# Kernel optimization log

Hardware: AMD Instinct MI355X
Metric: run time of the kernel (lower is better)

## Reference

```python
import jax, jax.numpy as jnp
import numpy as np

EPS_BN = 1e-5  # torch BatchNorm1d default eps
EPS_W = 1e-8   # dist reciprocal eps from source


def _bn_relu(x, gamma, beta):
    # x: [B, C, N]; training-mode batchnorm (biased var over B and N per channel)
    mean = jnp.mean(x, axis=(0, 2), keepdims=True)
    var = jnp.mean((x - mean) ** 2, axis=(0, 2), keepdims=True)
    xn = (x - mean) * jax.lax.rsqrt(var + EPS_BN)
    return jax.nn.relu(xn * gamma[None, :, None] + beta[None, :, None])


def setup_inputs() -> dict:
    key = jax.random.key(0)
    ks = jax.random.split(key, 12)
    B, N, S, D = 2, 16384, 4096, 256
    mlp = [256, 256]
    in_ch = 2 * D
    inp = {
        'xyz1': jax.random.normal(ks[0], (B, 3, N), jnp.float32),
        'xyz2': jax.random.normal(ks[1], (B, 3, S), jnp.float32),
        'points1': jax.random.normal(ks[2], (B, D, N), jnp.float32),
        'points2': jax.random.normal(ks[3], (B, D, S), jnp.float32),
    }
    last = in_ch
    for i, out in enumerate(mlp):
        inp[f'W{i}'] = jax.random.normal(ks[4 + 2 * i], (out, last), jnp.float32) * (1.0 / np.sqrt(last))
        inp[f'b{i}'] = jnp.zeros((out,), jnp.float32)
        inp[f'g{i}'] = jnp.ones((out,), jnp.float32)
        inp[f'be{i}'] = jnp.zeros((out,), jnp.float32)
        last = out
    return inp


def reference(xyz1, xyz2, points1, points2, W0, b0, g0, be0, W1, b1, g1, be1):
    B = xyz1.shape[0]
    p1 = jnp.swapaxes(xyz1, 1, 2)      # [B, N, 3]
    p2 = jnp.swapaxes(xyz2, 1, 2)      # [B, S, 3]
    f2 = jnp.swapaxes(points2, 1, 2)   # [B, S, D]

    # square_distance: ||a||^2 + ||b||^2 - 2 a.b  -> [B, N, S]
    d = (jnp.sum(p1 * p1, -1)[:, :, None]
         + jnp.sum(p2 * p2, -1)[:, None, :]
         - 2.0 * jnp.einsum('bnc,bsc->bns', p1, p2))

    # 3 nearest neighbors (same math as full sort + [:, :, :3])
    neg_top, idx = jax.lax.top_k(-d, 3)       # [B, N, 3]
    dists = -neg_top
    w = 1.0 / (dists + EPS_W)
    w = w / jnp.sum(w, axis=2, keepdims=True)  # [B, N, 3]

    # gather neighbor features: [B, N, 3, D]
    gathered = f2[jnp.arange(B)[:, None, None], idx]
    interp = jnp.sum(gathered * w[..., None], axis=2)   # [B, N, D]

    # concat skip features along channels -> [B, D1+D2, N]
    new_points = jnp.concatenate([points1, jnp.swapaxes(interp, 1, 2)], axis=1)

    # 1x1 conv + BN(train) + ReLU stack
    for W, b, g, be in ((W0, b0, g0, be0), (W1, b1, g1, be1)):
        new_points = _bn_relu(jnp.einsum('oc,bcn->bon', W, new_points) + b[None, :, None], g, be)
    return new_points
```

## Files before the change

kernel.cpp:

```cpp
#include <hip/hip_runtime.h>

#define NCHUNK 16

typedef __attribute__((ext_vector_type(8))) short bf16x8;
typedef __attribute__((ext_vector_type(4))) float f32x4;

__device__ __forceinline__ unsigned short f2bf(float f){
  union { float f; unsigned u; } v; v.f = f;
  unsigned u = v.u;
  u += 0x7FFFu + ((u >> 16) & 1u);
  return (unsigned short)(u >> 16);
}

__device__ __forceinline__ void gl_lds16(const void* g, void* l){
  __builtin_amdgcn_global_load_lds((const __attribute__((address_space(1))) unsigned*)g,
                                   (__attribute__((address_space(3))) unsigned*)l, 16, 0, 0);
}

__global__ __launch_bounds__(256) void k_convert_w(const float* __restrict__ W0, const float* __restrict__ W1,
                            unsigned short* __restrict__ W0b, unsigned short* __restrict__ W1b){
  int i = blockIdx.x*256 + threadIdx.x;
  if (i < 256*512) W0b[i] = f2bf(W0[i]);
  if (i < 256*256) W1b[i] = f2bf(W1[i]);
}

__global__ __launch_bounds__(256) void k_prep2(const float* __restrict__ xyz2, float* __restrict__ p2p){
  int i = blockIdx.x*256 + threadIdx.x;
  int b = i >> 12, s = i & 4095;
  const float* px = xyz2 + (size_t)b*3*4096;
  float x = px[s], y = px[4096+s], z = px[8192+s];
  float4 o; o.x = x; o.y = y; o.z = z; o.w = x*x + y*y + z*z;
  *(float4*)(p2p + (size_t)i*4) = o;
}

__global__ __launch_bounds__(256) void k_tp2(const float* __restrict__ p2, float* __restrict__ f2t){
  __shared__ float tile[64][65];
  int bx = blockIdx.x;
  int by = blockIdx.y;
  int b  = blockIdx.z;
  int t = threadIdx.x; int tx = t & 63; int ty = t >> 6;
  const float* src = p2 + ((size_t)b*256 + by*64)*4096 + bx*64;
  #pragma unroll
  for (int i = 0; i < 16; ++i){
    int c = ty*16 + i;
    tile[c][tx] = src[(size_t)c*4096 + tx];
  }
  __syncthreads();
  float* dst = f2t + ((size_t)b*4096 + (size_t)bx*64)*256 + by*64;
  #pragma unroll
  for (int i = 0; i < 16; ++i){
    int s = ty*16 + i;
    dst[(size_t)s*256 + tx] = tile[tx][s];
  }
}

__global__ __launch_bounds__(256) void k_tp1(const float* __restrict__ p1, unsigned short* __restrict__ Xt){
  __shared__ float tile[64][65];
  int bx = blockIdx.x;
  int by = blockIdx.y;
  int b  = blockIdx.z;
  int t = threadIdx.x; int tx = t & 63; int ty = t >> 6;
  const float* src = p1 + ((size_t)b*256 + by*64)*16384 + (size_t)bx*64;
  #pragma unroll
  for (int i = 0; i < 16; ++i){
    int c = ty*16 + i;
    tile[c][tx] = src[(size_t)c*16384 + tx];
  }
  __syncthreads();
  unsigned short* dst = Xt + ((size_t)b*16384 + (size_t)bx*64)*512 + by*64;
  #pragma unroll
  for (int i = 0; i < 16; ++i){
    int n = ty*16 + i;
    dst[(size_t)n*512 + tx] = f2bf(tile[tx][n]);
  }
}

__global__ __launch_bounds__(256) void k_knn(const float* __restrict__ xyz1, const float* __restrict__ p2p,
                      float* __restrict__ pd, int* __restrict__ pi){
  int b = blockIdx.z, cc = blockIdx.y;
  int n = blockIdx.x*256 + threadIdx.x;
  const float* q = xyz1 + (size_t)b*3*16384;
  float qx = q[n], qy = q[16384+n], qz = q[32768+n];
  float r1 = qx*qx + qy*qy + qz*qz;
  int s0 = cc*(4096/NCHUNK);
  const float4* cp = (const float4*)p2p + (size_t)b*4096 + s0;
  float d0=3.4e38f, d1=3.4e38f, d2=3.4e38f;
  int i0=0, i1=0, i2=0;
  #pragma unroll 16
  for (int j = 0; j < 4096/NCHUNK; ++j){
    float4 c = cp[j];
    float dot = qx*c.x + qy*c.y + qz*c.z;
    float d = (r1 + c.w) - 2.0f*dot;
    int s = s0 + j;
    bool c2 = d < d2, c1 = d < d1, c0 = d < d0;
    d2 = c1 ? d1 : (c2 ? d : d2);
    i2 = c1 ? i1 : (c2 ? s : i2);
    d1 = c1 ? (c0 ? d0 : d) : d1;
    i1 = c1 ? (c0 ? i0 : s) : i1;
    d0 = c0 ? d : d0;
    i0 = c0 ? s : i0;
  }
  size_t base = (((size_t)b*16384 + n)*NCHUNK + cc)*3;
  pd[base]=d0; pd[base+1]=d1; pd[base+2]=d2;
  pi[base]=i0; pi[base+1]=i1; pi[base+2]=i2;
}

__global__ __launch_bounds__(256) void k_knn_merge(const float* __restrict__ pd, const int* __restrict__ pi,
                            int* __restrict__ ki, float* __restrict__ kw){
  size_t qq = (size_t)blockIdx.x*256 + threadIdx.x;
  float d0=3.4e38f,d1=3.4e38f,d2=3.4e38f; int i0=0,i1=0,i2=0;
  size_t base = qq*NCHUNK*3;
  for (int c = 0; c < NCHUNK*3; ++c){
    float d = pd[base+c]; int s = pi[base+c];
    if (d < d2){
      if (d < d1){
        d2=d1; i2=i1;
        if (d < d0){ d1=d0; i1=i0; d0=d; i0=s; }
        else       { d1=d; i1=s; }
      } else { d2=d; i2=s; }
    }
  }
  float w0 = 1.0f/(d0+1e-8f), w1 = 1.0f/(d1+1e-8f), w2 = 1.0f/(d2+1e-8f);
  float inv = 1.0f/(w0+w1+w2);
  size_t kb = qq*3;
  ki[kb]=i0; ki[kb+1]=i1; ki[kb+2]=i2;
  kw[kb]=w0*inv; kw[kb+1]=w1*inv; kw[kb+2]=w2*inv;
}

__global__ __launch_bounds__(256) void k_interp(const float* __restrict__ f2t, const int* __restrict__ ki,
                         const float* __restrict__ kw, unsigned short* __restrict__ Xt){
  int t = threadIdx.x;
  int g = t >> 6; int lane = t & 63;
  size_t q = (size_t)blockIdx.x*4 + g;
  int b = (int)(q >> 14);
  const float* f2 = f2t + (size_t)b*4096*256;
  size_t kb = q*3;
  int i0 = ki[kb], i1 = ki[kb+1], i2 = ki[kb+2];
  float w0 = kw[kb], w1 = kw[kb+1], w2 = kw[kb+2];
  const float4 a = *(const float4*)(f2 + (size_t)i0*256 + lane*4);
  const float4 c = *(const float4*)(f2 + (size_t)i1*256 + lane*4);
  const float4 e = *(const float4*)(f2 + (size_t)i2*256 + lane*4);
  ushort4 o;
  o.x = f2bf(w0*a.x + w1*c.x + w2*e.x);
  o.y = f2bf(w0*a.y + w1*c.y + w2*e.y);
  o.z = f2bf(w0*a.z + w1*c.z + w2*e.z);
  o.w = f2bf(w0*a.w + w1*c.w + w2*e.w);
  *(ushort4*)(Xt + q*512 + 256 + lane*4) = o;
}

template<int K>
__global__ __launch_bounds__(256) void k_gemm(const unsigned short* __restrict__ A,
                       const unsigned short* __restrict__ Bm,
                       float* __restrict__ Ct,
                       float* __restrict__ psum, float* __restrict__ psq){
  __shared__ unsigned short As[128*32];
  __shared__ unsigned short Bs[128*32];
  __shared__ float redS[2][128];
  __shared__ float redQ[2][128];
  int t = threadIdx.x;
  int bo = blockIdx.x * 128;
  size_t bn = (size_t)blockIdx.y * 128;
  int w = t >> 6, l = t & 63;
  int wr = w >> 1, wc = w & 1;
  f32x4 acc[4][4] = {};

  const char* Ap = (const char*)A;
  const char* Bp = (const char*)Bm;
  int r0 = t >> 2;
  int cb = (t & 3) * 16;
  for (int k0 = 0; k0 < K; k0 += 32){
    __syncthreads();
    #pragma unroll
    for (int p = 0; p < 2; ++p){
      int off = (t + p*256)*16;
      int r = r0 + p*64;
      gl_lds16(Ap + (size_t)(bo + r)*(K*2) + (size_t)k0*2 + cb, (char*)As + off);
      gl_lds16(Bp + (bn + r)*(K*2) + (size_t)k0*2 + cb, (char*)Bs + off);
    }
    __syncthreads();
    bf16x8 af[4], bfr[4];
    int lr = l & 15, lk = (l >> 4) * 8;
    #pragma unroll
    for (int mt = 0; mt < 4; ++mt)
      af[mt] = *(const bf16x8*)(As + (wr*64 + mt*16 + lr)*32 + lk);
    #pragma unroll
    for (int nt = 0; nt < 4; ++nt)
      bfr[nt] = *(const bf16x8*)(Bs + (wc*64 + nt*16 + lr)*32 + lk);
    #pragma unroll
    for (int mt = 0; mt < 4; ++mt)
      #pragma unroll
      for (int nt = 0; nt < 4; ++nt)
        acc[mt][nt] = __builtin_amdgcn_mfma_f32_16x16x32_bf16(af[mt], bfr[nt], acc[mt][nt], 0, 0, 0);
  }
  int lo = (l >> 4) * 4, ln = l & 15;
  #pragma unroll
  for (int mt = 0; mt < 4; ++mt){
    #pragma unroll
    for (int nt = 0; nt < 4; ++nt){
      size_t n = bn + wc*64 + nt*16 + ln;
      int o = bo + wr*64 + mt*16 + lo;
      *(f32x4*)(Ct + n*256 + o) = acc[mt][nt];
    }
  }
  float ps[16], pq[16];
  #pragma unroll
  for (int mt = 0; mt < 4; ++mt){
    #pragma unroll
    for (int j = 0; j < 4; ++j){
      float s = 0.f, qv = 0.f;
      #pragma unroll
      for (int nt = 0; nt < 4; ++nt){
        float v = acc[mt][nt][j];
        s += v; qv += v*v;
      }
      ps[mt*4+j] = s; pq[mt*4+j] = qv;
    }
  }
  #pragma unroll
  for (int dlt = 1; dlt < 16; dlt <<= 1){
    #pragma unroll
    for (int i = 0; i < 16; ++i){
      ps[i] += __shfl_xor(ps[i], dlt);
      pq[i] += __shfl_xor(pq[i], dlt);
    }
  }
  if ((l & 15) == 0){
    #pragma unroll
    for (int mt = 0; mt < 4; ++mt){
      #pragma unroll
      for (int j = 0; j < 4; ++j){
        int ol = wr*64 + mt*16 + (l>>4)*4 + j;
        redS[wc][ol] = ps[mt*4+j];
        redQ[wc][ol] = pq[mt*4+j];
      }
    }
  }
  __syncthreads();
  if (t < 128){
    psum[(size_t)(bo + t)*256 + blockIdx.y] = redS[0][t] + redS[1][t];
    psq [(size_t)(bo + t)*256 + blockIdx.y] = redQ[0][t] + redQ[1][t];
  }
}

__global__ __launch_bounds__(256) void k_stats_f(const float* __restrict__ psum, const float* __restrict__ psq,
                          const float* __restrict__ gamma, const float* __restrict__ beta,
                          float* __restrict__ scale, float* __restrict__ shift){
  int o = blockIdx.x; int t = threadIdx.x;
  float s = psum[(size_t)o*256 + t];
  float q = psq [(size_t)o*256 + t];
  #pragma unroll
  for (int d = 1; d < 64; d <<= 1){
    s += __shfl_xor(s, d);
    q += __shfl_xor(q, d);
  }
  __shared__ float ls[4], lq[4];
  if ((t & 63) == 0){ ls[t>>6] = s; lq[t>>6] = q; }
  __syncthreads();
  if (t == 0){
    float S = ls[0]+ls[1]+ls[2]+ls[3];
    float Q = lq[0]+lq[1]+lq[2]+lq[3];
    const float invc = 1.0f/32768.0f;
    float mean = S*invc;
    float var = Q*invc - mean*mean;
    float sc = gamma[o]*rsqrtf(var + 1e-5f);
    scale[o] = sc;
    shift[o] = beta[o] - mean*sc;
  }
}

__global__ __launch_bounds__(256) void k_apply_y(const float* __restrict__ C, const float* __restrict__ scale,
                          const float* __restrict__ shift, unsigned short* __restrict__ Y){
  size_t i = (size_t)blockIdx.x*256 + threadIdx.x;
  float4 v = *(const float4*)(C + i*4);
  int c = (int)((i*4) & 255);
  ushort4 o;
  o.x = f2bf(fmaxf(0.f, v.x*scale[c]   + shift[c]));
  o.y = f2bf(fmaxf(0.f, v.y*scale[c+1] + shift[c+1]));
  o.z = f2bf(fmaxf(0.f, v.z*scale[c+2] + shift[c+2]));
  o.w = f2bf(fmaxf(0.f, v.w*scale[c+3] + shift[c+3]));
  *(ushort4*)(Y + i*4) = o;
}

__global__ __launch_bounds__(256) void k_bn_out(const float* __restrict__ C, const float* __restrict__ scale,
                         const float* __restrict__ shift, float* __restrict__ out){
  __shared__ float tile[64][65];
  int bx = blockIdx.x;
  int by = blockIdx.y;
  int b  = blockIdx.z;
  int t = threadIdx.x; int tx = t & 63; int ty = t >> 6;
  const float* src = C + ((size_t)b*16384 + (size_t)bx*64)*256 + by*64;
  int o = by*64 + tx;
  float sc = scale[o], sh = shift[o];
  #pragma unroll
  for (int i = 0; i < 16; ++i){
    int n = ty*16 + i;
    float v = src[(size_t)n*256 + tx];
    tile[n][tx] = fmaxf(0.f, v*sc + sh);
  }
  __syncthreads();
  float* dst = out + ((size_t)b*256 + by*64)*16384 + (size_t)bx*64;
  #pragma unroll
  for (int i = 0; i < 16; ++i){
    int oo = ty*16 + i;
    dst[(size_t)oo*16384 + tx] = tile[tx][oo];
  }
}

extern "C" void kernel_launch(void* const* d_in, const int* in_sizes, int n_in,
                              void* d_out, int out_size, void* d_ws, size_t ws_size,
                              hipStream_t stream){
  const float* xyz1    = (const float*)d_in[0];
  const float* xyz2    = (const float*)d_in[1];
  const float* points1 = (const float*)d_in[2];
  const float* points2 = (const float*)d_in[3];
  const float* W0  = (const float*)d_in[4];
  const float* g0  = (const float*)d_in[6];
  const float* be0 = (const float*)d_in[7];
  const float* W1  = (const float*)d_in[8];
  const float* g1  = (const float*)d_in[10];
  const float* be1 = (const float*)d_in[11];

  char* w = (char*)d_ws;
  size_t o = 0;
  float* f2t = (float*)(w + o); o += 8388608;
  float* p2p = (float*)(w + o); o += 131072;
  int*   kidx= (int*)(w + o);   o += 393216;
  float* kww = (float*)(w + o); o += 393216;
  unsigned short* W0b = (unsigned short*)(w + o); o += 262144;
  unsigned short* W1b = (unsigned short*)(w + o); o += 131072;
  float* psum = (float*)(w + o); o += 262144;
  float* psq  = (float*)(w + o); o += 262144;
  float* scale1 = (float*)(w + o); o += 1024;
  float* shift1 = (float*)(w + o); o += 1024;
  float* scale2 = (float*)(w + o); o += 1024;
  float* shift2 = (float*)(w + o); o += 1024;
  unsigned short* Xt = (unsigned short*)(w + o); size_t xto = o; o += 33554432;
  float* C1t = (float*)(w + o); size_t c1o = o; o += 33554432;
  unsigned short* Yt = (unsigned short*)(w + o); o += 16777216;
  float* C2t = (float*)(w + xto);
  float* kpd = (float*)(w + c1o);
  int*   kpi = (int*)(w + c1o + 6291456);

  k_convert_w<<<512, 256, 0, stream>>>(W0, W1, W0b, W1b);
  k_prep2<<<32, 256, 0, stream>>>(xyz2, p2p);
  k_tp2<<<dim3(64,4,2), 256, 0, stream>>>(points2, f2t);
  k_knn<<<dim3(64,NCHUNK,2), 256, 0, stream>>>(xyz1, p2p, kpd, kpi);
  k_knn_merge<<<128, 256, 0, stream>>>(kpd, kpi, kidx, kww);
  k_tp1<<<dim3(256,4,2), 256, 0, stream>>>(points1, Xt);
  k_interp<<<8192, 256, 0, stream>>>(f2t, kidx, kww, Xt);
  k_gemm<512><<<dim3(2,256), 256, 0, stream>>>(W0b, Xt, C1t, psum, psq);
  k_stats_f<<<256, 256, 0, stream>>>(psum, psq, g0, be0, scale1, shift1);
  k_apply_y<<<8192, 256, 0, stream>>>(C1t, scale1, shift1, Yt);
  k_gemm<256><<<dim3(2,256), 256, 0, stream>>>(W1b, Yt, C2t, psum, psq);
  k_stats_f<<<256, 256, 0, stream>>>(psum, psq, g1, be1, scale2, shift2);
  k_bn_out<<<dim3(256,4,2), 256, 0, stream>>>(C2t, scale2, shift2, (float*)d_out);
}
```

Before: 185.6 us.

## Store GEMM outputs as bf16, simplify KNN top-3 update, fuse prep kernel

The GEMM epilogues now write their pre-BN activations as bf16 instead of fp32. This halves the write traffic of both GEMMs and the read traffic of the apply and output kernels, and the workspace layout is reorganised to match. Batch statistics are still accumulated from the fp32 accumulators, but normalisation is applied to rounded values, which adds a small precision loss. The KNN top-3 insertion is rewritten with min/max chains to cut select instructions, and the xyz2 prep kernel is folded into the weight conversion kernel to save one launch.

```diff
diff --git a/kernel.cpp b/kernel.cpp
--- a/kernel.cpp
+++ b/kernel.cpp
@@ -12,25 +12,29 @@
   return (unsigned short)(u >> 16);
 }
 
+__device__ __forceinline__ float bf2f(unsigned short h){
+  union { unsigned u; float f; } v; v.u = ((unsigned)h) << 16;
+  return v.f;
+}
+
 __device__ __forceinline__ void gl_lds16(const void* g, void* l){
   __builtin_amdgcn_global_load_lds((const __attribute__((address_space(1))) unsigned*)g,
                                    (__attribute__((address_space(3))) unsigned*)l, 16, 0, 0);
 }
 
 __global__ __launch_bounds__(256) void k_convert_w(const float* __restrict__ W0, const float* __restrict__ W1,
-                            unsigned short* __restrict__ W0b, unsigned short* __restrict__ W1b){
+                            unsigned short* __restrict__ W0b, unsigned short* __restrict__ W1b,
+                            const float* __restrict__ xyz2, float* __restrict__ p2p){
   int i = blockIdx.x*256 + threadIdx.x;
   if (i < 256*512) W0b[i] = f2bf(W0[i]);
   if (i < 256*256) W1b[i] = f2bf(W1[i]);
-}
-
-__global__ __launch_bounds__(256) void k_prep2(const float* __restrict__ xyz2, float* __restrict__ p2p){
-  int i = blockIdx.x*256 + threadIdx.x;
-  int b = i >> 12, s = i & 4095;
-  const float* px = xyz2 + (size_t)b*3*4096;
-  float x = px[s], y = px[4096+s], z = px[8192+s];
-  float4 o; o.x = x; o.y = y; o.z = z; o.w = x*x + y*y + z*z;
-  *(float4*)(p2p + (size_t)i*4) = o;
+  if (i < 8192){
+    int b = i >> 12, s = i & 4095;
+    const float* px = xyz2 + (size_t)b*3*4096;
+    float x = px[s], y = px[4096+s], z = px[8192+s];
+    float4 o; o.x = x; o.y = y; o.z = z; o.w = x*x + y*y + z*z;
+    *(float4*)(p2p + (size_t)i*4) = o;
+  }
 }
 
 __global__ __launch_bounds__(256) void k_tp2(const float* __restrict__ p2, float* __restrict__ f2t){
@@ -84,7 +88,7 @@
   float r1 = qx*qx + qy*qy + qz*qz;
   int s0 = cc*(4096/NCHUNK);
   const float4* cp = (const float4*)p2p + (size_t)b*4096 + s0;
-  float d0=3.4e38f, d1=3.4e38f, d2=3.4e38f;
+  float m0=3.4e38f, m1=3.4e38f, m2=3.4e38f;
   int i0=0, i1=0, i2=0;
   #pragma unroll 16
   for (int j = 0; j < 4096/NCHUNK; ++j){
@@ -92,16 +96,20 @@
     float dot = qx*c.x + qy*c.y + qz*c.z;
     float d = (r1 + c.w) - 2.0f*dot;
     int s = s0 + j;
-    bool c2 = d < d2, c1 = d < d1, c0 = d < d0;
-    d2 = c1 ? d1 : (c2 ? d : d2);
-    i2 = c1 ? i1 : (c2 ? s : i2);
-    d1 = c1 ? (c0 ? d0 : d) : d1;
-    i1 = c1 ? (c0 ? i0 : s) : i1;
-    d0 = c0 ? d : d0;
-    i0 = c0 ? s : i0;
+    bool c0 = d < m0, c1 = d < m1, c2 = d < m2;
+    float t1 = fmaxf(m0, d);
+    m0 = fminf(m0, d);
+    float t2 = fmaxf(m1, t1);
+    m1 = fminf(m1, t1);
+    m2 = fminf(m2, t2);
+    int j1 = c0 ? i0 : s;
+    int j2 = c1 ? i1 : s;
+    i0 = c0 ? s  : i0;
+    i1 = c1 ? j1 : i1;
+    i2 = c2 ? j2 : i2;
   }
   size_t base = (((size_t)b*16384 + n)*NCHUNK + cc)*3;
-  pd[base]=d0; pd[base+1]=d1; pd[base+2]=d2;
+  pd[base]=m0; pd[base+1]=m1; pd[base+2]=m2;
   pi[base]=i0; pi[base+1]=i1; pi[base+2]=i2;
 }
 
@@ -151,7 +159,7 @@
 template<int K>
 __global__ __launch_bounds__(256) void k_gemm(const unsigned short* __restrict__ A,
                        const unsigned short* __restrict__ Bm,
-                       float* __restrict__ Ct,
+                       unsigned short* __restrict__ Cb,
                        float* __restrict__ psum, float* __restrict__ psq){
   __shared__ unsigned short As[128*32];
   __shared__ unsigned short Bs[128*32];
@@ -199,7 +207,10 @@
     for (int nt = 0; nt < 4; ++nt){
       size_t n = bn + wc*64 + nt*16 + ln;
       int o = bo + wr*64 + mt*16 + lo;
-      *(f32x4*)(Ct + n*256 + o) = acc[mt][nt];
+      ushort4 ov;
+      ov.x = f2bf(acc[mt][nt][0]); ov.y = f2bf(acc[mt][nt][1]);
+      ov.z = f2bf(acc[mt][nt][2]); ov.w = f2bf(acc[mt][nt][3]);
+      *(ushort4*)(Cb + n*256 + o) = ov;
     }
   }
   float ps[16], pq[16];
@@ -268,33 +279,33 @@
   }
 }
 
-__global__ __launch_bounds__(256) void k_apply_y(const float* __restrict__ C, const float* __restrict__ scale,
+__global__ __launch_bounds__(256) void k_apply_y(const unsigned short* __restrict__ Cb, const float* __restrict__ scale,
                           const float* __restrict__ shift, unsigned short* __restrict__ Y){
   size_t i = (size_t)blockIdx.x*256 + threadIdx.x;
-  float4 v = *(const float4*)(C + i*4);
+  ushort4 v = *(const ushort4*)(Cb + i*4);
   int c = (int)((i*4) & 255);
   ushort4 o;
-  o.x = f2bf(fmaxf(0.f, v.x*scale[c]   + shift[c]));
-  o.y = f2bf(fmaxf(0.f, v.y*scale[c+1] + shift[c+1]));
-  o.z = f2bf(fmaxf(0.f, v.z*scale[c+2] + shift[c+2]));
-  o.w = f2bf(fmaxf(0.f, v.w*scale[c+3] + shift[c+3]));
+  o.x = f2bf(fmaxf(0.f, bf2f(v.x)*scale[c]   + shift[c]));
+  o.y = f2bf(fmaxf(0.f, bf2f(v.y)*scale[c+1] + shift[c+1]));
+  o.z = f2bf(fmaxf(0.f, bf2f(v.z)*scale[c+2] + shift[c+2]));
+  o.w = f2bf(fmaxf(0.f, bf2f(v.w)*scale[c+3] + shift[c+3]));
   *(ushort4*)(Y + i*4) = o;
 }
 
-__global__ __launch_bounds__(256) void k_bn_out(const float* __restrict__ C, const float* __restrict__ scale,
+__global__ __launch_bounds__(256) void k_bn_out(const unsigned short* __restrict__ Cb, const float* __restrict__ scale,
                          const float* __restrict__ shift, float* __restrict__ out){
   __shared__ float tile[64][65];
   int bx = blockIdx.x;
   int by = blockIdx.y;
   int b  = blockIdx.z;
   int t = threadIdx.x; int tx = t & 63; int ty = t >> 6;
-  const float* src = C + ((size_t)b*16384 + (size_t)bx*64)*256 + by*64;
+  const unsigned short* src = Cb + ((size_t)b*16384 + (size_t)bx*64)*256 + by*64;
   int o = by*64 + tx;
   float sc = scale[o], sh = shift[o];
   #pragma unroll
   for (int i = 0; i < 16; ++i){
     int n = ty*16 + i;
-    float v = src[(size_t)n*256 + tx];
+    float v = bf2f(src[(size_t)n*256 + tx]);
     tile[n][tx] = fmaxf(0.f, v*sc + sh);
   }
   __syncthreads();
@@ -334,24 +345,23 @@
   float* shift1 = (float*)(w + o); o += 1024;
   float* scale2 = (float*)(w + o); o += 1024;
   float* shift2 = (float*)(w + o); o += 1024;
+  float* kpd = (float*)(w + o); o += 6291456;
+  int*   kpi = (int*)(w + o);   o += 6291456;
   unsigned short* Xt = (unsigned short*)(w + o); size_t xto = o; o += 33554432;
-  float* C1t = (float*)(w + o); size_t c1o = o; o += 33554432;
-  unsigned short* Yt = (unsigned short*)(w + o); o += 16777216;
-  float* C2t = (float*)(w + xto);
-  float* kpd = (float*)(w + c1o);
-  int*   kpi = (int*)(w + c1o + 6291456);
-
-  k_convert_w<<<512, 256, 0, stream>>>(W0, W1, W0b, W1b);
-  k_prep2<<<32, 256, 0, stream>>>(xyz2, p2p);
+  unsigned short* C1b = (unsigned short*)(w + o); o += 16777216;
+  unsigned short* Yt  = (unsigned short*)(w + o); o += 16777216;
+  unsigned short* C2b = (unsigned short*)(w + xto);
+
+  k_convert_w<<<512, 256, 0, stream>>>(W0, W1, W0b, W1b, xyz2, p2p);
   k_tp2<<<dim3(64,4,2), 256, 0, stream>>>(points2, f2t);
   k_knn<<<dim3(64,NCHUNK,2), 256, 0, stream>>>(xyz1, p2p, kpd, kpi);
   k_knn_merge<<<128, 256, 0, stream>>>(kpd, kpi, kidx, kww);
   k_tp1<<<dim3(256,4,2), 256, 0, stream>>>(points1, Xt);
   k_interp<<<8192, 256, 0, stream>>>(f2t, kidx, kww, Xt);
-  k_gemm<512><<<dim3(2,256), 256, 0, stream>>>(W0b, Xt, C1t, psum, psq);
+  k_gemm<512><<<dim3(2,256), 256, 0, stream>>>(W0b, Xt, C1b, psum, psq);
   k_stats_f<<<256, 256, 0, stream>>>(psum, psq, g0, be0, scale1, shift1);
-  k_apply_y<<<8192, 256, 0, stream>>>(C1t, scale1, shift1, Yt);
-  k_gemm<256><<<dim3(2,256), 256, 0, stream>>>(W1b, Yt, C2t, psum, psq);
+  k_apply_y<<<8192, 256, 0, stream>>>(C1b, scale1, shift1, Yt);
+  k_gemm<256><<<dim3(2,256), 256, 0, stream>>>(W1b, Yt, C2b, psum, psq);
   k_stats_f<<<256, 256, 0, stream>>>(psum, psq, g1, be1, scale2, shift2);
-  k_bn_out<<<dim3(256,4,2), 256, 0, stream>>>(C2t, scale2, shift2, (float*)d_out);
-}
+  k_bn_out<<<dim3(256,4,2), 256, 0, stream>>>(C2b, scale2, shift2, (float*)d_out);
+}
```

Result: faster. 178.7 us (-3.7%).
